# Kernel tuning notes

Hardware: AMD Instinct MI355X
Metric: run time of the kernel (lower is better)

The kernel has to match this reference:

```python
import jax, jax.numpy as jnp
import numpy as np

EPS = 1e-5

def _sqnorm(x):
    return jnp.sum(x * x, axis=-1, keepdims=True)

def _norm(x):
    return jnp.sqrt(_sqnorm(x) + 1e-15)

def _artanh(x):
    return jnp.arctanh(jnp.clip(x, -1.0 + EPS, 1.0 - EPS))

def exp0(v):
    n = _norm(v)
    return jnp.tanh(n) * v / jnp.maximum(n, EPS)

def log0(x):
    n = jnp.clip(_norm(x), EPS, 1.0 - EPS)
    return _artanh(n) * x / n

def mob_scalar(x, r):
    n = jnp.clip(_norm(x), EPS, 1.0 - EPS)
    return jnp.tanh(r * _artanh(n)) * x / n

def mob_add(x, y):
    x2 = _sqnorm(x); y2 = _sqnorm(y)
    xy = jnp.sum(x * y, axis=-1, keepdims=True)
    num = (1.0 + 2.0 * xy + y2) * x + (1.0 - x2) * y
    den = 1.0 + 2.0 * xy + x2 * y2
    return num / jnp.maximum(den, EPS)

def pdist(x, y):
    # Poincare-ball geodesic distance, keepdims on last axis
    d2 = _sqnorm(x - y)
    den = jnp.maximum((1.0 - _sqnorm(x)) * (1.0 - _sqnorm(y)), EPS)
    return jnp.arccosh(jnp.maximum(1.0 + 2.0 * d2 / den, 1.0 + 1e-7))

def _coattention(D, Q, q1):
    # vectorized form of the per-slot loop: each slot i reads the ORIGINAL D[:, i]
    Dd = jax.lax.stop_gradient(D)                       # Zk_s is detached in torch
    # [N, F_D, F_Q, 1] attention over Q neighbors for every D slot
    G = jax.nn.softmax(-pdist(Dd[:, :, None, :], Q[:, None, :, :]), axis=2)
    nh = exp0(jnp.sum(log0(mob_scalar(Q[:, None, :, :], G)), axis=2))  # [N, F_D, d]
    return mob_add(mob_scalar(Dd, q1), nh)

def _aggregate(h_self, h_neigh, scalar):
    att = jax.nn.softmax(-pdist(h_self[:, None, :], h_neigh), axis=1)  # [N, F, 1]
    nTE = exp0(jnp.sum(log0(mob_scalar(h_neigh, att)), axis=1))        # [N, d]
    return mob_add(mob_scalar(h_self, scalar), nTE)

def _mode_forward(x, D_idx, Q_idx, emb0, emb1, win, bin_, q, qq, q1, aw1, ab1, aw2, wout, bout):
    f = jnp.concatenate([emb0[x[:, 0]], emb1[x[:, 1]]], axis=-1)  # [N, 64]
    f = exp0(f @ win + bin_)
    D = f[D_idx]; Q = f[Q_idx]                                    # [N, F, d]
    h_neigh = _coattention(D, Q, q1)
    e1 = _aggregate(f, h_neigh, q)
    e2 = _aggregate(f, Q, qq)
    z = jnp.stack([log0(e1), log0(e2)], axis=1)                   # [N, 2, d]
    beta = jax.nn.softmax(jnp.tanh(z @ aw1 + ab1) @ aw2, axis=1)  # [N, 2, 1]
    rst = exp0(jnp.sum(beta * z, axis=1))
    return exp0(log0(rst) @ wout + bout)

N, F, DH, V0, V1 = 2048, 20, 64, 100000, 1000

def setup_inputs() -> dict:
    key = jax.random.key(0)
    ks = jax.random.split(key, 32)
    def mk(k, shape, s=0.1):
        return (jax.random.normal(k, shape) * s).astype(jnp.float32)
    inp = {
        'x': jax.random.randint(ks[0], (N, 2), 0, V1).astype(jnp.int32),
        'idx_sim': jax.random.randint(ks[1], (N, F), 0, N).astype(jnp.int32),
        'idx_cor': jax.random.randint(ks[2], (N, F), 0, N).astype(jnp.int32),
    }
    for mi, m in enumerate(['sim', 'cor']):
        kk = jax.random.split(ks[3 + mi], 12)
        inp[f'emb0_{m}'] = mk(kk[0], (V0, 32))
        inp[f'emb1_{m}'] = mk(kk[1], (V1, 32))
        inp[f'win_{m}'] = mk(kk[2], (64, DH))
        inp[f'bin_{m}'] = mk(kk[3], (DH,))
        inp[f'q_{m}'] = jnp.full((1,), 0.1, jnp.float32)
        inp[f'qq_{m}'] = jnp.full((1,), 0.1, jnp.float32)
        inp[f'q1_{m}'] = jnp.full((1,), 0.1, jnp.float32)
        inp[f'aw1_{m}'] = mk(kk[4], (64, 32))
        inp[f'ab1_{m}'] = mk(kk[5], (32,))
        inp[f'aw2_{m}'] = mk(kk[6], (32, 1))
        inp[f'wout_{m}'] = mk(kk[7], (DH, 64))
        inp[f'bout_{m}'] = mk(kk[8], (64,))
    return inp

def reference(x, idx_sim, idx_cor,
              emb0_sim, emb1_sim, win_sim, bin_sim, q_sim, qq_sim, q1_sim,
              aw1_sim, ab1_sim, aw2_sim, wout_sim, bout_sim,
              emb0_cor, emb1_cor, win_cor, bin_cor, q_cor, qq_cor, q1_cor,
              aw1_cor, ab1_cor, aw2_cor, wout_cor, bout_cor):
    # mode 'sim': D = feat[idx_cor], Q = feat[idx_sim]; mode 'cor': swapped
    out_sim = _mode_forward(x, idx_cor, idx_sim, emb0_sim, emb1_sim, win_sim, bin_sim,
                            q_sim, qq_sim, q1_sim, aw1_sim, ab1_sim, aw2_sim, wout_sim, bout_sim)
    out_cor = _mode_forward(x, idx_sim, idx_cor, emb0_cor, emb1_cor, win_cor, bin_cor,
                            q_cor, qq_cor, q1_cor, aw1_cor, ab1_cor, aw2_cor, wout_cor, bout_cor)
    return jnp.stack([out_sim, out_cor], axis=0)  # [2, N, 64]
```

## Files before the change

kernel.cpp:

```cpp
#include <hip/hip_runtime.h>

#define EPS 1e-5f
#define ONE_M_EPS (1.0f - 1e-5f)
#define NROW 2048
#define FF 20
#define DH 64
#define PADW (DH + 4)
#define NPAIR (FF * FF)
#define NPAIR2 (NPAIR + FF)

typedef float v2f __attribute__((ext_vector_type(2)));

__device__ __forceinline__ float frcp(float x) { return __builtin_amdgcn_rcpf(x); }
__device__ __forceinline__ float fsq(float x) { return __builtin_amdgcn_sqrtf(x); }
__device__ __forceinline__ v2f pkfma(v2f a, v2f b, v2f c) {
  return __builtin_elementwise_fma(a, b, c);
}
__device__ __forceinline__ float rdlane(float v, int lane) {
  return __int_as_float(__builtin_amdgcn_readlane(__float_as_int(v), lane));
}

template <int CTRL>
__device__ __forceinline__ float dppadd(float x) {
  int t = __builtin_amdgcn_update_dpp(0, __float_as_int(x), CTRL, 0xf, 0xf, false);
  return x + __int_as_float(t);
}
__device__ __forceinline__ float wredb(float v) {
  v = dppadd<0x111>(v);
  v = dppadd<0x112>(v);
  v = dppadd<0x114>(v);
  v = dppadd<0x118>(v);
  v = dppadd<0x142>(v);
  v = dppadd<0x143>(v);
  return rdlane(v, 63);
}

__device__ __forceinline__ float ftanh(float x) {
  float ax = fabsf(x);
  float e = __expf(-2.f * ax);
  float t = (1.f - e) * frcp(1.f + e);
  return copysignf(t, x);
}

__device__ __forceinline__ float ftanhp(float x) {
  float e = __expf(-2.f * x);
  return (1.f - e) * frcp(1.f + e);
}

__device__ __forceinline__ float fatanh(float x) {
  return 0.5f * __logf((1.f + x) * frcp(1.f - x));
}

__device__ __forceinline__ float clampn(float x) {
  return fminf(fmaxf(x, EPS), ONE_M_EPS);
}

__device__ __forceinline__ float expnacosh(float arg) {
  return frcp(arg + fsq(fmaxf(arg * arg - 1.f, 0.f)));
}

__device__ __forceinline__ float dot64(const float* __restrict__ a,
                                       const float* __restrict__ b) {
  const float4* ap = (const float4*)a;
  const float4* bp = (const float4*)b;
  v2f acc = {0.f, 0.f};
#pragma unroll
  for (int kk = 0; kk < DH / 4; ++kk) {
    float4 x = ap[kk];
    float4 y = bp[kk];
    acc = pkfma(v2f{x.x, x.y}, v2f{y.x, y.y}, acc);
    acc = pkfma(v2f{x.z, x.w}, v2f{y.z, y.w}, acc);
  }
  return acc.x + acc.y;
}

struct FeatParams {
  const float *emb0, *emb1, *win, *bin;
  float* fout;
};

struct ModeParams {
  const float* f;
  const int *Didx, *Qidx;
  const float *q1p, *qp, *qqp, *aw1, *ab1, *aw2, *wout, *bout;
  float* out;
};

__global__ __launch_bounds__(64) void feat_kernel(const int* __restrict__ x,
                                                  FeatParams ps, FeatParams pc) {
  const int bid = blockIdx.x;
  const int mode = bid >= NROW;
  const FeatParams P = mode ? pc : ps;
  const int n = bid - mode * NROW;
  const int l = threadIdx.x;
  __shared__ float u[DH];
  int x0 = x[n * 2 + 0];
  int x1 = x[n * 2 + 1];
  u[l] = (l < 32) ? P.emb0[x0 * 32 + l] : P.emb1[x1 * 32 + (l - 32)];
  __syncthreads();
  v2f acc2 = {P.bin[l], 0.f};
#pragma unroll
  for (int k = 0; k < DH; k += 2) {
    v2f uv = *(const v2f*)&u[k];
    v2f wv = {P.win[k * DH + l], P.win[(k + 1) * DH + l]};
    acc2 = pkfma(uv, wv, acc2);
  }
  float acc = acc2.x + acc2.y;
  float a2 = wredb(acc * acc);
  float nn = fsq(a2 + 1e-15f);
  P.fout[n * DH + l] = ftanhp(nn) * frcp(fmaxf(nn, EPS)) * acc;
}

__global__ __launch_bounds__(256) void mode_kernel(ModeParams pm0,
                                                   ModeParams pm1) {
  const int bid = blockIdx.x;
  const int mode = bid >= NROW;
  const ModeParams P = mode ? pm1 : pm0;
  const int n = bid - mode * NROW;
  const int tid = threadIdx.x;
  const int l = tid & 63;
  const int w = tid >> 6;

  __shared__ alignas(16) float Ds[FF][PADW];
  __shared__ alignas(16) float Qs[FF][PADW];
  __shared__ alignas(16) float fs_[PADW];
  __shared__ alignas(16) float Gm[NPAIR];
  __shared__ float Fq[FF];
  __shared__ float D2[FF];
  __shared__ float FD[FF], X2s[FF];
  __shared__ float Q2[FF], WQ[FF];
  __shared__ float C1[FF], C2[FF], WH[FF];
  __shared__ float zb[2][DH];
  __shared__ float ub[DH];
  __shared__ float pb[4][DH];

  float (*As)[PADW] = Qs;

  const float* f = P.f;
  float fv = f[n * DH + l];

  for (int i = w; i < FF; i += 4) {
    Ds[i][l] = f[P.Didx[n * FF + i] * DH + l];
    Qs[i][l] = f[P.Qidx[n * FF + i] * DH + l];
  }
  if (w == 0) fs_[l] = fv;
  float f2 = wredb(fv * fv);
  float fnc = clampn(fsq(f2 + 1e-15f));
  float fA = fatanh(fnc);
  float q1 = P.q1p[0], qsc = P.qp[0], qqsc = P.qqp[0];
  __syncthreads();

  if (w < 2 && l < FF) {
    const float* rp = (w == 0) ? &Ds[l][0] : &Qs[l][0];
    float dot = dot64(rp, rp);
    float nc = clampn(fsq(dot + 1e-15f));
    float at = fatanh(nc);
    if (w == 0) {
      D2[l] = dot;
      float fd = ftanh(q1 * at) * frcp(nc);
      FD[l] = fd;
      X2s[l] = fd * fd * dot;
    } else {
      Q2[l] = dot;
      WQ[l] = at * frcp(nc);
    }
  }
  __syncthreads();

  float qregS[FF];
#pragma unroll
  for (int j = 0; j < FF; ++j) qregS[j] = WQ[j] * Qs[j][l];

  for (int p = tid; p < NPAIR2; p += 256) {
    int i = p / FF;
    int j = p - i * FF;
    const float* ap = (i < FF) ? &Ds[i][0] : &fs_[0];
    float dot = dot64(ap, &Qs[j][0]);
    if (i < FF) {
      float d2 = D2[i] + Q2[j] - 2.f * dot;
      float den = fmaxf((1.f - D2[i]) * (1.f - Q2[j]), EPS);
      float arg = fmaxf(1.f + 2.f * d2 * frcp(den), 1.f + 1e-7f);
      Gm[p] = expnacosh(arg);
    } else {
      Fq[j] = dot;
    }
  }
  __syncthreads();

  float acc5[5];
#pragma unroll
  for (int s = 0; s < 5; ++s) {
    const int i = w + 4 * s;
    const float4* gr = (const float4*)(&Gm[i * FF]);
    v2f ss2 = {0.f, 0.f};
    v2f ac2 = {0.f, 0.f};
#pragma unroll
    for (int jq = 0; jq < FF / 4; ++jq) {
      float4 g4 = gr[jq];
      ss2 += v2f{g4.x, g4.y} + v2f{g4.z, g4.w};
      ac2 = pkfma(v2f{g4.x, g4.y}, v2f{qregS[4 * jq + 0], qregS[4 * jq + 1]},
                  ac2);
      ac2 = pkfma(v2f{g4.z, g4.w}, v2f{qregS[4 * jq + 2], qregS[4 * jq + 3]},
                  ac2);
    }
    float acc = (ac2.x + ac2.y) * frcp(ss2.x + ss2.y);
    acc5[s] = acc;
    As[i][l] = acc;
  }
  __syncthreads();

  if (w == 0) {
    const bool isA = (l < FF);
    const bool isX = (l >= 32 && l < 32 + FF);
    const float* pa = isA ? &As[l][0] : (isX ? &As[l - 32][0] : &fs_[0]);
    const float* pc2 = isA ? &As[l][0] : (isX ? &Ds[l - 32][0] : &fs_[0]);
    float dotv = dot64(pa, pc2);
    float xyv = __shfl(dotv, l + 32, 64);
    if (isA) {
      float a2 = dotv;
      float xy0 = xyv;
      float nn = fsq(a2 + 1e-15f);
      float ec = ftanhp(nn) * frcp(fmaxf(nn, EPS));
      float fDc = FD[l];
      float x2 = X2s[l];
      float y2 = ec * ec * a2;
      float xy = fDc * ec * xy0;
      float al = 1.f + 2.f * xy + y2;
      float be = 1.f - x2;
      float rd = frcp(fmaxf(1.f + 2.f * xy + x2 * y2, EPS));
      C1[l] = al * fDc * rd;
      C2[l] = be * ec * rd;
      float h2 = (al * al * x2 + 2.f * al * be * xy + be * be * y2) * rd * rd;
      D2[l] = h2;
      float nc = clampn(fsq(h2 + 1e-15f));
      WH[l] = fatanh(nc) * frcp(nc);
    }
  }
  __syncthreads();

#pragma unroll
  for (int s = 0; s < 5; ++s) {
    const int i = w + 4 * s;
    Ds[i][l] = fmaf(C1[i], Ds[i][l], C2[i] * acc5[s]);
  }
  __syncthreads();

  if (w < 2) {
    float a1 = 0.f;
    float wh = 1.f;
    if (w == 0) {
      if (l < FF) {
        float h2 = D2[l];
        wh = WH[l];
        float dot = dot64(&fs_[0], &Ds[l][0]);
        float d2 = f2 + h2 - 2.f * dot;
        float den = fmaxf((1.f - f2) * (1.f - h2), EPS);
        float arg = fmaxf(1.f + 2.f * d2 * frcp(den), 1.f + 1e-7f);
        a1 = expnacosh(arg);
      }
    } else {
      if (l < FF) {
        float d2 = f2 + Q2[l] - 2.f * Fq[l];
        float den = fmaxf((1.f - f2) * (1.f - Q2[l]), EPS);
        float arg = fmaxf(1.f + 2.f * d2 * frcp(den), 1.f + 1e-7f);
        a1 = expnacosh(arg);
      }
    }
    float s = wredb(a1);
    float c = (l < FF) ? a1 * frcp(s) * wh : 0.f;
    float accE = 0.f;
    if (w == 0) {
#pragma unroll
      for (int j = 0; j < FF; ++j) accE = fmaf(rdlane(c, j), Ds[j][l], accE);
    } else {
#pragma unroll
      for (int j = 0; j < FF; ++j) accE = fmaf(rdlane(c, j), qregS[j], accE);
    }
    float a2 = wredb(accE * accE);
    float nn = fsq(a2 + 1e-15f);
    float ec = ftanhp(nn) * frcp(fmaxf(nn, EPS));
    float nTE = ec * accE;
    float r = (w == 0) ? qsc : qqsc;
    float fsc = ftanh(r * fA) * frcp(fnc);
    float xv = fsc * fv;
    float x2 = fsc * fsc * f2;
    float y2 = ec * ec * a2;
    float xy = wredb(xv * nTE);
    float al = 1.f + 2.f * xy + y2;
    float be = 1.f - x2;
    float rd = frcp(fmaxf(1.f + 2.f * xy + x2 * y2, EPS));
    float ev = (al * xv + be * nTE) * rd;
    float es = (al * al * x2 + 2.f * al * be * xy + be * be * y2) * rd * rd;
    float n1 = clampn(fsq(es + 1e-15f));
    zb[w][l] = fatanh(n1) * frcp(n1) * ev;
  }
  __syncthreads();

  if (w == 0) {
    int p_ = l >> 5, c_ = l & 31;
    v2f mm2 = {P.ab1[c_], 0.f};
#pragma unroll
    for (int k = 0; k < DH; k += 2) {
      v2f zv = *(const v2f*)&zb[p_][k];
      v2f av = {P.aw1[k * 32 + c_], P.aw1[(k + 1) * 32 + c_]};
      mm2 = pkfma(zv, av, mm2);
    }
    float tt = ftanh(mm2.x + mm2.y);
    float sr = tt * P.aw2[c_];
    sr = dppadd<0x111>(sr);
    sr = dppadd<0x112>(sr);
    sr = dppadd<0x114>(sr);
    sr = dppadd<0x118>(sr);
    sr = dppadd<0x142>(sr);
    float s0 = rdlane(sr, 31);
    float s1 = rdlane(sr, 63);
    float bm = fmaxf(s0, s1);
    float b0 = __expf(s0 - bm), b1 = __expf(s1 - bm);
    float bi = frcp(b0 + b1);
    b0 *= bi;
    b1 *= bi;
    float rv = fmaf(b0, zb[0][l], b1 * zb[1][l]);
    float r2 = wredb(rv * rv);
    float rn = fsq(r2 + 1e-15f);
    float sc = ftanhp(rn) * frcp(fmaxf(rn, EPS));
    float rst = sc * rv;
    float rr = sc * sc * r2;
    float rc = clampn(fsq(rr + 1e-15f));
    ub[l] = fatanh(rc) * frcp(rc) * rst;
  }
  __syncthreads();

  {
    v2f oo2 = {0.f, 0.f};
#pragma unroll
    for (int k = 0; k < DH / 4; k += 2) {
      int kk = w * (DH / 4) + k;
      v2f uv = *(const v2f*)&ub[kk];
      v2f wv = {P.wout[kk * DH + l], P.wout[(kk + 1) * DH + l]};
      oo2 = pkfma(uv, wv, oo2);
    }
    pb[w][l] = oo2.x + oo2.y;
  }
  __syncthreads();
  if (w == 0) {
    float oo = P.bout[l] + ((pb[0][l] + pb[1][l]) + (pb[2][l] + pb[3][l]));
    float o2 = wredb(oo * oo);
    float on = fsq(o2 + 1e-15f);
    P.out[n * DH + l] = ftanhp(on) * frcp(fmaxf(on, EPS)) * oo;
  }
}

extern "C" void kernel_launch(void* const* d_in, const int* in_sizes, int n_in,
                              void* d_out, int out_size, void* d_ws,
                              size_t ws_size, hipStream_t stream) {
  const int* x = (const int*)d_in[0];
  const int* idx_sim = (const int*)d_in[1];
  const int* idx_cor = (const int*)d_in[2];
  const float* p[2][12];
  for (int m = 0; m < 2; ++m)
    for (int k = 0; k < 12; ++k) p[m][k] = (const float*)d_in[3 + m * 12 + k];

  float* fsim = (float*)d_ws;
  float* fcor = fsim + NROW * DH;
  float* out = (float*)d_out;

  FeatParams fps = {p[0][0], p[0][1], p[0][2], p[0][3], fsim};
  FeatParams fpc = {p[1][0], p[1][1], p[1][2], p[1][3], fcor};
  feat_kernel<<<2 * NROW, 64, 0, stream>>>(x, fps, fpc);

  ModeParams m0 = {fsim, idx_cor, idx_sim, p[0][6], p[0][4], p[0][5],
                   p[0][7], p[0][8], p[0][9], p[0][10], p[0][11], out};
  ModeParams m1 = {fcor, idx_sim, idx_cor, p[1][6], p[1][4], p[1][5],
                   p[1][7], p[1][8], p[1][9], p[1][10], p[1][11], out + NROW * DH};
  mode_kernel<<<2 * NROW, 256, 0, stream>>>(m0, m1);
}
```

Measured before the change: 42.61 us.

## Use fp16 dot2 for pairwise distance dots and single-wave output projection

Keeps half-precision copies of the gathered D, Q and self rows in shared memory and computes the 420 pairwise dot products with fdot2 instructions, halving LDS traffic for that phase. The output projection now runs on one wave over all 64 inputs, which removes the partial-sum buffer and one block barrier. The fp32 dot helper also gets two independent accumulators to shorten its dependency chain. The fp16 dots lose precision in d2 = |D|^2 + |Q|^2 - 2·dot, which can hurt accuracy for nearby points, and the single-wave projection serialises more work onto one wave.

```diff
diff --git a/kernel.cpp b/kernel.cpp
--- a/kernel.cpp
+++ b/kernel.cpp
@@ -6,10 +6,12 @@
 #define FF 20
 #define DH 64
 #define PADW (DH + 4)
+#define PADH 72
 #define NPAIR (FF * FF)
 #define NPAIR2 (NPAIR + FF)
 
 typedef float v2f __attribute__((ext_vector_type(2)));
+typedef _Float16 v2h __attribute__((ext_vector_type(2)));
 
 __device__ __forceinline__ float frcp(float x) { return __builtin_amdgcn_rcpf(x); }
 __device__ __forceinline__ float fsq(float x) { return __builtin_amdgcn_sqrtf(x); }
@@ -63,15 +65,37 @@
                                        const float* __restrict__ b) {
   const float4* ap = (const float4*)a;
   const float4* bp = (const float4*)b;
-  v2f acc = {0.f, 0.f};
+  v2f accA = {0.f, 0.f}, accB = {0.f, 0.f};
 #pragma unroll
   for (int kk = 0; kk < DH / 4; ++kk) {
     float4 x = ap[kk];
     float4 y = bp[kk];
-    acc = pkfma(v2f{x.x, x.y}, v2f{y.x, y.y}, acc);
-    acc = pkfma(v2f{x.z, x.w}, v2f{y.z, y.w}, acc);
-  }
+    accA = pkfma(v2f{x.x, x.y}, v2f{y.x, y.y}, accA);
+    accB = pkfma(v2f{x.z, x.w}, v2f{y.z, y.w}, accB);
+  }
+  v2f acc = accA + accB;
   return acc.x + acc.y;
+}
+
+__device__ __forceinline__ float dot64h(const _Float16* __restrict__ a,
+                                        const _Float16* __restrict__ b) {
+  const uint4* ap = (const uint4*)a;
+  const uint4* bp = (const uint4*)b;
+  float acc0 = 0.f, acc1 = 0.f;
+#pragma unroll
+  for (int kk = 0; kk < 8; ++kk) {
+    uint4 x = ap[kk];
+    uint4 y = bp[kk];
+    acc0 = __builtin_amdgcn_fdot2(__builtin_bit_cast(v2h, x.x),
+                                  __builtin_bit_cast(v2h, y.x), acc0, false);
+    acc1 = __builtin_amdgcn_fdot2(__builtin_bit_cast(v2h, x.y),
+                                  __builtin_bit_cast(v2h, y.y), acc1, false);
+    acc0 = __builtin_amdgcn_fdot2(__builtin_bit_cast(v2h, x.z),
+                                  __builtin_bit_cast(v2h, y.z), acc0, false);
+    acc1 = __builtin_amdgcn_fdot2(__builtin_bit_cast(v2h, x.w),
+                                  __builtin_bit_cast(v2h, y.w), acc1, false);
+  }
+  return acc0 + acc1;
 }
 
 struct FeatParams {
@@ -124,6 +148,9 @@
   __shared__ alignas(16) float Ds[FF][PADW];
   __shared__ alignas(16) float Qs[FF][PADW];
   __shared__ alignas(16) float fs_[PADW];
+  __shared__ alignas(16) _Float16 Dh[FF][PADH];
+  __shared__ alignas(16) _Float16 Qh[FF][PADH];
+  __shared__ alignas(16) _Float16 fh[PADH];
   __shared__ alignas(16) float Gm[NPAIR];
   __shared__ float Fq[FF];
   __shared__ float D2[FF];
@@ -132,7 +159,6 @@
   __shared__ float C1[FF], C2[FF], WH[FF];
   __shared__ float zb[2][DH];
   __shared__ float ub[DH];
-  __shared__ float pb[4][DH];
 
   float (*As)[PADW] = Qs;
 
@@ -140,10 +166,17 @@
   float fv = f[n * DH + l];
 
   for (int i = w; i < FF; i += 4) {
-    Ds[i][l] = f[P.Didx[n * FF + i] * DH + l];
-    Qs[i][l] = f[P.Qidx[n * FF + i] * DH + l];
-  }
-  if (w == 0) fs_[l] = fv;
+    float dv = f[P.Didx[n * FF + i] * DH + l];
+    float qv = f[P.Qidx[n * FF + i] * DH + l];
+    Ds[i][l] = dv;
+    Qs[i][l] = qv;
+    Dh[i][l] = (_Float16)dv;
+    Qh[i][l] = (_Float16)qv;
+  }
+  if (w == 0) {
+    fs_[l] = fv;
+    fh[l] = (_Float16)fv;
+  }
   float f2 = wredb(fv * fv);
   float fnc = clampn(fsq(f2 + 1e-15f));
   float fA = fatanh(fnc);
@@ -174,8 +207,8 @@
   for (int p = tid; p < NPAIR2; p += 256) {
     int i = p / FF;
     int j = p - i * FF;
-    const float* ap = (i < FF) ? &Ds[i][0] : &fs_[0];
-    float dot = dot64(ap, &Qs[j][0]);
+    const _Float16* ap = (i < FF) ? &Dh[i][0] : &fh[0];
+    float dot = dot64h(ap, &Qh[j][0]);
     if (i < FF) {
       float d2 = D2[i] + Q2[j] - 2.f * dot;
       float den = fmaxf((1.f - D2[i]) * (1.f - Q2[j]), EPS);
@@ -330,20 +363,15 @@
   }
   __syncthreads();
 
-  {
+  if (w == 0) {
     v2f oo2 = {0.f, 0.f};
 #pragma unroll
-    for (int k = 0; k < DH / 4; k += 2) {
-      int kk = w * (DH / 4) + k;
-      v2f uv = *(const v2f*)&ub[kk];
-      v2f wv = {P.wout[kk * DH + l], P.wout[(kk + 1) * DH + l]};
+    for (int k = 0; k < DH; k += 2) {
+      v2f uv = *(const v2f*)&ub[k];
+      v2f wv = {P.wout[k * DH + l], P.wout[(k + 1) * DH + l]};
       oo2 = pkfma(uv, wv, oo2);
     }
-    pb[w][l] = oo2.x + oo2.y;
-  }
-  __syncthreads();
-  if (w == 0) {
-    float oo = P.bout[l] + ((pb[0][l] + pb[1][l]) + (pb[2][l] + pb[3][l]));
+    float oo = P.bout[l] + oo2.x + oo2.y;
     float o2 = wredb(oo * oo);
     float on = fsq(o2 + 1e-15f);
     P.out[n * DH + l] = ftanhp(on) * frcp(fmaxf(on, EPS)) * oo;
```

Result: no change. 41.82 us (-1.9%).
